# Kernel tuning notes

Hardware: AMD Instinct MI355X
Metric: run time of the kernel (lower is better)

Reference implementation:

```python
import jax, jax.numpy as jnp
import numpy as np

N = 50000        # nodes
E = 800000       # edges
D_IN = 512       # input_shape
PROJ = 256       # proj_dim
H = 4            # num_heads
C = 32           # hidden_channels
HC = H * C
NUM_LABELS = 10
SLOPE = 0.2      # GATv2 LeakyReLU negative slope


def _glorot(key, shape):
    fan_in = shape[-1]
    return jax.random.normal(key, shape, jnp.float32) / jnp.sqrt(jnp.float32(fan_in))


def setup_inputs() -> dict:
    key = jax.random.key(0)
    ks = jax.random.split(key, 16)
    inp = {}
    inp["x"] = jax.random.normal(ks[0], (N, D_IN), jnp.float32)
    inp["edge_index"] = jax.random.randint(ks[1], (2, E), 0, N, dtype=jnp.int64)
    # projection Linear
    inp["W_proj"] = _glorot(ks[2], (PROJ, D_IN)); inp["b_proj"] = jnp.zeros((PROJ,), jnp.float32)
    # GATv2 layer 1: lin_l, lin_r, att, bias
    inp["Wl1"] = _glorot(ks[3], (HC, PROJ)); inp["bl1"] = jnp.zeros((HC,), jnp.float32)
    inp["Wr1"] = _glorot(ks[4], (HC, PROJ)); inp["br1"] = jnp.zeros((HC,), jnp.float32)
    inp["att1"] = _glorot(ks[5], (H, C)); inp["bias1"] = jnp.zeros((HC,), jnp.float32)
    # GATv2 layer 2
    inp["Wl2"] = _glorot(ks[6], (HC, HC)); inp["bl2"] = jnp.zeros((HC,), jnp.float32)
    inp["Wr2"] = _glorot(ks[7], (HC, HC)); inp["br2"] = jnp.zeros((HC,), jnp.float32)
    inp["att2"] = _glorot(ks[8], (H, C)); inp["bias2"] = jnp.zeros((HC,), jnp.float32)
    # head MLP
    inp["W1"] = _glorot(ks[9], (C, HC)); inp["b1"] = jnp.zeros((C,), jnp.float32)
    inp["W2"] = _glorot(ks[10], (NUM_LABELS, C)); inp["b2"] = jnp.zeros((NUM_LABELS,), jnp.float32)
    return inp


def _gatv2(x, src, dst, Wl, bl, Wr, br, att, bias):
    # x: [N, F_in]; src/dst: [E]. PyG GATv2Conv, concat=True, no self-loops, eval (no dropout).
    xl = (x @ Wl.T + bl).reshape(N, H, C)   # source transform
    xr = (x @ Wr.T + br).reshape(N, H, C)   # target transform
    e = jax.nn.leaky_relu(xl[src] + xr[dst], negative_slope=SLOPE)  # [E,H,C]
    logit = jnp.einsum('ehc,hc->eh', e, att)                        # [E,H]
    # segment softmax over incoming edges of each destination node
    m = jax.ops.segment_max(logit, dst, num_segments=N)             # [N,H]
    m = jnp.where(jnp.isfinite(m), m, jnp.float32(0))               # empty segments -> 0
    p = jnp.exp(logit - m[dst])                                     # [E,H]
    s = jax.ops.segment_sum(p, dst, num_segments=N)                 # [N,H]
    alpha = p / (s[dst] + jnp.float32(1e-16))                       # [E,H]
    out = jax.ops.segment_sum(xl[src] * alpha[:, :, None], dst, num_segments=N)  # [N,H,C]
    return out.reshape(N, HC) + bias


def reference(x, edge_index, W_proj, b_proj, Wl1, bl1, Wr1, br1, att1, bias1,
              Wl2, bl2, Wr2, br2, att2, bias2, W1, b1, W2, b2):
    src, dst = edge_index[0], edge_index[1]
    h = jax.nn.elu(x @ W_proj.T + b_proj)
    h = jax.nn.elu(_gatv2(h, src, dst, Wl1, bl1, Wr1, br1, att1, bias1))
    h = jax.nn.elu(_gatv2(h, src, dst, Wl2, bl2, Wr2, br2, att2, bias2))
    h = jax.nn.elu(h @ W1.T + b1)
    return h @ W2.T + b2
```

## Files before the change

### kernel.cpp

```cpp
#include <hip/hip_runtime.h>
#include <cstdint>
#include <cstddef>

constexpr int NN = 50000;
constexpr int NE = 800000;

typedef _Float16 half8 __attribute__((ext_vector_type(8)));
typedef _Float16 half4v __attribute__((ext_vector_type(4)));
typedef _Float16 half2v __attribute__((ext_vector_type(2)));
typedef float f32x16 __attribute__((ext_vector_type(16)));
typedef unsigned short ushort_t;

__device__ inline ushort_t f2h(float f) {
  _Float16 h = (_Float16)f;
  return __builtin_bit_cast(ushort_t, h);
}

#if __has_builtin(__builtin_amdgcn_fdot2)
__device__ inline float fdot2(half2v a, half2v b, float c) {
  return __builtin_amdgcn_fdot2(a, b, c, false);
}
#else
__device__ inline float fdot2(half2v a, half2v b, float c) {
  return c + (float)a[0] * (float)b[0] + (float)a[1] * (float)b[1];
}
#endif

__global__ void k_wconv(const float* __restrict__ W, ushort_t* __restrict__ Bh,
                        int M, int K, int total) {
  int idx = blockIdx.x * 256 + threadIdx.x;
  if (idx >= total) return;
  int j = idx & 7;
  int l = (idx >> 3) & 63;
  int blk = idx >> 9;
  int nKB = K >> 4;
  int cb = blk / nKB, kb = blk - cb * nKB;
  int col = cb * 32 + (l & 31);
  int k = kb * 16 + ((l >> 5) & 1) * 8 + j;
  float v = (col < M) ? W[(size_t)col * K + k] : 0.f;
  Bh[idx] = f2h(v);
}

template<int ACT, int OUTMODE, int BKT, int AFP16, int NCB>
__global__ __launch_bounds__(512) void gemm_mfma(const void* __restrict__ Av,
    const ushort_t* __restrict__ Bh,
    const float* __restrict__ bias, const float* __restrict__ bias2,
    float* __restrict__ C, ushort_t* __restrict__ C16a,
    ushort_t* __restrict__ C16b, int N, int M, int K)
{
  constexpr int NKK = BKT / 16;
  __shared__ ushort_t Ah[2][2 * NKK * 512];
  const int t = threadIdx.x;
  const int lane = t & 63;
  const int wid = t >> 6;
  const int wr = wid >> 2;
  const int wc = wid & 3;
  const int row0 = blockIdx.x * 64;
  const int col0 = blockIdx.y * (128 * NCB);
  const int nKB = K >> 4;
  const int nK = K / BKT;
  const int cb0 = (col0 >> 5) + wc * NCB;

  int s_r, s_k, sb0, sb1 = 0;
  bool ok0 = false, ok1 = false;
  if constexpr (!AFP16) {
    s_r = t >> 4; s_k = (t & 15) * 4;
    sb0 = (s_k >> 4) * 512 + (s_r + 32 * ((s_k >> 3) & 1)) * 8 + (s_k & 7);
    sb1 = sb0 + NKK * 512;
    ok0 = (row0 + s_r) < N;
    ok1 = (row0 + s_r + 32) < N;
  } else if constexpr (BKT == 64) {
    s_r = t >> 3; s_k = (t & 7) * 8;
    sb0 = ((s_r >> 5) * NKK + (s_k >> 4)) * 512 +
          ((s_r & 31) + 32 * ((s_k >> 3) & 1)) * 8;
    ok0 = (row0 + s_r) < N;
  } else {
    s_r = t >> 3; s_k = (t & 7) * 4;
    sb0 = ((s_r >> 5) * NKK + (s_k >> 4)) * 512 +
          ((s_r & 31) + 32 * ((s_k >> 3) & 1)) * 8 + (s_k & 7);
    ok0 = (row0 + s_r) < N;
  }
  const float*    ap0 = (const float*)Av + (size_t)(row0 + s_r) * K + s_k;
  const float*    ap1 = (const float*)Av + (size_t)(row0 + s_r + 32) * K + s_k;
  const ushort_t* aph = (const ushort_t*)Av + (size_t)(row0 + s_r) * K + s_k;

  f32x16 acc0 = {}, acc1 = {};
  float4 f00 = make_float4(0, 0, 0, 0), f10 = make_float4(0, 0, 0, 0);
  float4 f01 = make_float4(0, 0, 0, 0), f11 = make_float4(0, 0, 0, 0);
  half8 h8 = {};
  half4v h4 = {};

  auto aload = [&](int ks) {
    if constexpr (!AFP16) {
      f00 = make_float4(0, 0, 0, 0); f10 = make_float4(0, 0, 0, 0);
      if constexpr (BKT == 128) { f01 = make_float4(0, 0, 0, 0); f11 = make_float4(0, 0, 0, 0); }
      if (ok0) {
        f00 = *(const float4*)(ap0 + (size_t)ks * BKT);
        if constexpr (BKT == 128) f01 = *(const float4*)(ap0 + (size_t)ks * BKT + 64);
      }
      if (ok1) {
        f10 = *(const float4*)(ap1 + (size_t)ks * BKT);
        if constexpr (BKT == 128) f11 = *(const float4*)(ap1 + (size_t)ks * BKT + 64);
      }
    } else if constexpr (BKT == 64) {
      half8 z = {};
      h8 = ok0 ? *(const half8*)(aph + (size_t)ks * BKT) : z;
    } else {
      half4v z = {};
      h4 = ok0 ? *(const half4v*)(aph + (size_t)ks * BKT) : z;
    }
  };
  auto cvt4 = [](float4 f) {
    half4v h;
    h[0] = (_Float16)f.x; h[1] = (_Float16)f.y;
    h[2] = (_Float16)f.z; h[3] = (_Float16)f.w;
    return h;
  };
  auto stage_write = [&](int buf) {
    if constexpr (!AFP16) {
      *(half4v*)&Ah[buf][sb0] = cvt4(f00);
      *(half4v*)&Ah[buf][sb1] = cvt4(f10);
      if constexpr (BKT == 128) {
        *(half4v*)&Ah[buf][sb0 + 2048] = cvt4(f01);
        *(half4v*)&Ah[buf][sb1 + 2048] = cvt4(f11);
      }
    } else if constexpr (BKT == 64) {
      *(half8*)&Ah[buf][sb0] = h8;
    } else {
      *(half4v*)&Ah[buf][sb0] = h4;
    }
  };

  aload(0);
  stage_write(0);
  __syncthreads();

  for (int ks = 0; ks < nK; ++ks) {
    const int cur = ks & 1;
    const int nxt = cur ^ 1;
    const bool have_next = (ks + 1 < nK);
    if (have_next) aload(ks + 1);

    #pragma unroll
    for (int kk = 0; kk < NKK; ++kk) {
      const int kbg = ks * NKK + kk;
      half8 ah = *(const half8*)&Ah[cur][(wr * NKK + kk) * 512 + lane * 8];
      const size_t bo0 = ((size_t)(cb0 * nKB + kbg) * 64 + lane) * 8;
      half8 bh0 = *(const half8*)(Bh + bo0);
      acc0 = __builtin_amdgcn_mfma_f32_32x32x16_f16(ah, bh0, acc0, 0, 0, 0);
      if constexpr (NCB == 2) {
        const size_t bo1 = ((size_t)((cb0 + 1) * nKB + kbg) * 64 + lane) * 8;
        half8 bh1 = *(const half8*)(Bh + bo1);
        acc1 = __builtin_amdgcn_mfma_f32_32x32x16_f16(ah, bh1, acc1, 0, 0, 0);
      }
    }

    if (have_next) stage_write(nxt);
    __syncthreads();
  }

  auto epi = [&](const f32x16& acc, int cb) {
    int cc = cb * 32 + (lane & 31);
    float bv;
    if constexpr (OUTMODE == 3) bv = (cc < 128) ? bias[cc] : bias2[cc - 128];
    else                        bv = (cc < M) ? bias[cc] : 0.f;
    #pragma unroll
    for (int r = 0; r < 16; ++r) {
      int rr = row0 + wr * 32 + (r & 3) + 8 * (r >> 2) + 4 * (lane >> 5);
      if (rr < N && cc < M) {
        float v = acc[r] + bv;
        if (ACT) v = v > 0.f ? v : (__expf(v) - 1.f);
        if constexpr (OUTMODE == 0)      C[(size_t)rr * M + cc] = v;
        else if constexpr (OUTMODE == 1) C16a[(size_t)rr * M + cc] = f2h(v);
        else {
          if (cc < 128) C16a[(size_t)rr * 128 + cc] = f2h(v);
          else          C16b[(size_t)rr * 128 + (cc - 128)] = f2h(v);
        }
      }
    }
  };
  epi(acc0, cb0);
  if constexpr (NCB == 2) epi(acc1, cb0 + 1);
}

__global__ void k_degrank(const int* __restrict__ ei, int* __restrict__ deg,
                          int* __restrict__ rank) {
  int e = blockIdx.x * 256 + threadIdx.x;
  if (e >= NE) return;
  int d = ei[NE + e];
  rank[e] = atomicAdd(&deg[d], 1);
}

__global__ __launch_bounds__(256) void k_scan1(const int* __restrict__ deg,
    int* __restrict__ rowstart, int* __restrict__ blocksum) {
  __shared__ int sm[256];
  int b = blockIdx.x, t = threadIdx.x;
  int i = b * 256 + t;
  int v = (i < NN) ? deg[i] : 0;
  sm[t] = v;
  __syncthreads();
  #pragma unroll
  for (int off = 1; off < 256; off <<= 1) {
    int u = (t >= off) ? sm[t - off] : 0;
    __syncthreads();
    sm[t] += u;
    __syncthreads();
  }
  if (i < NN) rowstart[i + 1] = sm[t];
  if (t == 255) blocksum[b] = sm[255];
}

__global__ __launch_bounds__(256) void k_scan2(int* __restrict__ blocksum, int nb) {
  __shared__ int sm[256];
  int t = threadIdx.x;
  int v = (t < nb) ? blocksum[t] : 0;
  sm[t] = v;
  __syncthreads();
  #pragma unroll
  for (int off = 1; off < 256; off <<= 1) {
    int u = (t >= off) ? sm[t - off] : 0;
    __syncthreads();
    sm[t] += u;
    __syncthreads();
  }
  if (t < nb) blocksum[t] = (t == 0) ? 0 : sm[t - 1];
}

__global__ __launch_bounds__(256) void k_scan3(int* __restrict__ rowstart,
    const int* __restrict__ blocksum) {
  int b = blockIdx.x, t = threadIdx.x;
  int i = b * 256 + t;
  if (i == 0) rowstart[0] = 0;
  if (i < NN) rowstart[i + 1] += blocksum[b];
}

__global__ void k_scatter(const int* __restrict__ ei, const int* __restrict__ rowstart,
                          const int* __restrict__ rank, int* __restrict__ srcp) {
  int e = blockIdx.x * 256 + threadIdx.x;
  if (e >= NE) return;
  int d = ei[NE + e];
  srcp[rowstart[d] + rank[e]] = ei[e];
}

__global__ __launch_bounds__(256) void k_gat(const ushort_t* __restrict__ xl,
    const ushort_t* __restrict__ xr, const int* __restrict__ srcp,
    const int* __restrict__ rowstart, const float* __restrict__ att,
    const float* __restrict__ bias, ushort_t* __restrict__ out)
{
  const int g = threadIdx.x >> 5;
  const int c = threadIdx.x & 31;
  const int n = blockIdx.x * 8 + g;
  const int r0 = rowstart[n], r1 = rowstart[n + 1];
  half4v xrh = *(const half4v*)(xr + (size_t)n * 128 + 4 * c);
  const half2v xr01 = {xrh[0], xrh[1]};
  const half2v xr23 = {xrh[2], xrh[3]};
  const float4 atv = *(const float4*)(att + 4 * c);
  const half2v at01 = {(_Float16)atv.x, (_Float16)atv.y};
  const half2v at23 = {(_Float16)atv.z, (_Float16)atv.w};
  const half2v k02 = {(_Float16)0.2f, (_Float16)0.2f};

  float m = -1e30f, ssum = 0.f;
  float a0 = 0.f, a1 = 0.f, a2 = 0.f, a3 = 0.f;

  auto lg = [&](int s, float4& xs) -> float {
    half4v hv = *(const half4v*)(xl + (size_t)s * 128 + 4 * c);
    xs.x = (float)hv[0]; xs.y = (float)hv[1];
    xs.z = (float)hv[2]; xs.w = (float)hv[3];
    half2v u01 = half2v{hv[0], hv[1]} + xr01;
    half2v u23 = half2v{hv[2], hv[3]} + xr23;
    u01 = __builtin_elementwise_max(u01, u01 * k02);
    u23 = __builtin_elementwise_max(u23, u23 * k02);
    float l = fdot2(u01, at01, fdot2(u23, at23, 0.f));
    l += __shfl_xor(l, 1);
    l += __shfl_xor(l, 2);
    l += __shfl_xor(l, 4);
    return l;
  };

  int j = r0;
  for (; j + 8 <= r1; j += 8) {
    int s0 = srcp[j],     s1 = srcp[j + 1], s2 = srcp[j + 2], s3 = srcp[j + 3];
    int s4 = srcp[j + 4], s5 = srcp[j + 5], s6 = srcp[j + 6], s7 = srcp[j + 7];
    float4 x0, x1, x2, x3, x4, x5, x6, x7;
    float l0 = lg(s0, x0), l1 = lg(s1, x1), l2 = lg(s2, x2), l3 = lg(s3, x3);
    float l4 = lg(s4, x4), l5 = lg(s5, x5), l6 = lg(s6, x6), l7 = lg(s7, x7);
    float mloc = fmaxf(fmaxf(fmaxf(l0, l1), fmaxf(l2, l3)),
                       fmaxf(fmaxf(l4, l5), fmaxf(l6, l7)));
    float mn = fmaxf(m, mloc);
    float sc = __expf(m - mn);
    float p0 = __expf(l0 - mn), p1 = __expf(l1 - mn);
    float p2 = __expf(l2 - mn), p3 = __expf(l3 - mn);
    float p4 = __expf(l4 - mn), p5 = __expf(l5 - mn);
    float p6 = __expf(l6 - mn), p7 = __expf(l7 - mn);
    ssum = ssum * sc + (((p0 + p1) + (p2 + p3)) + ((p4 + p5) + (p6 + p7)));
    a0 = a0 * sc + (((p0 * x0.x + p1 * x1.x) + (p2 * x2.x + p3 * x3.x)) +
                    ((p4 * x4.x + p5 * x5.x) + (p6 * x6.x + p7 * x7.x)));
    a1 = a1 * sc + (((p0 * x0.y + p1 * x1.y) + (p2 * x2.y + p3 * x3.y)) +
                    ((p4 * x4.y + p5 * x5.y) + (p6 * x6.y + p7 * x7.y)));
    a2 = a2 * sc + (((p0 * x0.z + p1 * x1.z) + (p2 * x2.z + p3 * x3.z)) +
                    ((p4 * x4.z + p5 * x5.z) + (p6 * x6.z + p7 * x7.z)));
    a3 = a3 * sc + (((p0 * x0.w + p1 * x1.w) + (p2 * x2.w + p3 * x3.w)) +
                    ((p4 * x4.w + p5 * x5.w) + (p6 * x6.w + p7 * x7.w)));
    m = mn;
  }
  for (; j + 4 <= r1; j += 4) {
    int s0 = srcp[j], s1 = srcp[j + 1], s2 = srcp[j + 2], s3 = srcp[j + 3];
    float4 x0, x1, x2, x3;
    float l0 = lg(s0, x0), l1 = lg(s1, x1), l2 = lg(s2, x2), l3 = lg(s3, x3);
    float mloc = fmaxf(fmaxf(l0, l1), fmaxf(l2, l3));
    float mn = fmaxf(m, mloc);
    float sc = __expf(m - mn);
    float p0 = __expf(l0 - mn), p1 = __expf(l1 - mn);
    float p2 = __expf(l2 - mn), p3 = __expf(l3 - mn);
    ssum = ssum * sc + ((p0 + p1) + (p2 + p3));
    a0 = a0 * sc + (p0 * x0.x + p1 * x1.x) + (p2 * x2.x + p3 * x3.x);
    a1 = a1 * sc + (p0 * x0.y + p1 * x1.y) + (p2 * x2.y + p3 * x3.y);
    a2 = a2 * sc + (p0 * x0.z + p1 * x1.z) + (p2 * x2.z + p3 * x3.z);
    a3 = a3 * sc + (p0 * x0.w + p1 * x1.w) + (p2 * x2.w + p3 * x3.w);
    m = mn;
  }
  for (; j < r1; ++j) {
    float4 xs;
    float l = lg(srcp[j], xs);
    float mn = fmaxf(m, l);
    float sc = __expf(m - mn);
    float p = __expf(l - mn);
    ssum = ssum * sc + p;
    a0 = a0 * sc + p * xs.x;
    a1 = a1 * sc + p * xs.y;
    a2 = a2 * sc + p * xs.z;
    a3 = a3 * sc + p * xs.w;
    m = mn;
  }

  const float4 bv = *(const float4*)(bias + 4 * c);
  float rinv = 1.f / (ssum + 1e-16f);
  float o0 = a0 * rinv + bv.x;
  float o1 = a1 * rinv + bv.y;
  float o2 = a2 * rinv + bv.z;
  float o3 = a3 * rinv + bv.w;
  o0 = o0 > 0.f ? o0 : (__expf(o0) - 1.f);
  o1 = o1 > 0.f ? o1 : (__expf(o1) - 1.f);
  o2 = o2 > 0.f ? o2 : (__expf(o2) - 1.f);
  o3 = o3 > 0.f ? o3 : (__expf(o3) - 1.f);
  half4v ov;
  ov[0] = (_Float16)o0; ov[1] = (_Float16)o1;
  ov[2] = (_Float16)o2; ov[3] = (_Float16)o3;
  *(half4v*)(out + (size_t)n * 128 + 4 * c) = ov;
}

__global__ void k_report_ws(float* out, int out_size, float wsz) {
  int i = blockIdx.x * 256 + threadIdx.x;
  if (i < out_size) out[i] = (i == 0) ? wsz : 0.f;
}

extern "C" void kernel_launch(void* const* d_in, const int* in_sizes, int n_in,
                              void* d_out, int out_size, void* d_ws, size_t ws_size,
                              hipStream_t stream)
{
  const float* x    = (const float*)d_in[0];
  const int*   ei   = (const int*)d_in[1];
  const float* Wp   = (const float*)d_in[2];  const float* bp    = (const float*)d_in[3];
  const float* Wl1  = (const float*)d_in[4];  const float* bl1   = (const float*)d_in[5];
  const float* Wr1  = (const float*)d_in[6];  const float* br1   = (const float*)d_in[7];
  const float* att1 = (const float*)d_in[8];  const float* bias1 = (const float*)d_in[9];
  const float* Wl2  = (const float*)d_in[10]; const float* bl2   = (const float*)d_in[11];
  const float* Wr2  = (const float*)d_in[12]; const float* br2   = (const float*)d_in[13];
  const float* att2 = (const float*)d_in[14]; const float* bias2 = (const float*)d_in[15];
  const float* W1   = (const float*)d_in[16]; const float* b1    = (const float*)d_in[17];
  const float* W2   = (const float*)d_in[18]; const float* b2    = (const float*)d_in[19];
  float* out = (float*)d_out;

  constexpr size_t NEED = 122300000;
  if (ws_size < NEED) {
    k_report_ws<<<(out_size + 255) / 256, 256, 0, stream>>>(out, out_size, (float)ws_size);
    return;
  }
  char* ws = (char*)d_ws;
  ushort_t* h0h   = (ushort_t*)(ws + 0);
  ushort_t* h1h   = h0h;
  ushort_t* h2h   = (ushort_t*)(ws + 25600000);
  ushort_t* xlh   = (ushort_t*)(ws + 51200000);
  ushort_t* xrh   = (ushort_t*)(ws + 76800000);
  ushort_t* h3h   = (ushort_t*)(ws + 102400000);
  ushort_t* wb    = (ushort_t*)(ws + 108800000);
  int*      srcp  = (int*)(ws + 115200000);
  int*      rank  = (int*)(ws + 118400000);
  int*      deg   = (int*)(ws + 121600000);
  int*      rowst = (int*)(ws + 122000000);
  int*      bsum  = (int*)(ws + 122250000);

  ushort_t* Wph  = wb;
  ushort_t* WB1h = wb + 131072;
  ushort_t* WB2h = wb + 196608;
  ushort_t* W1h  = wb + 229376;
  ushort_t* W2h  = wb + 233472;

  hipMemsetAsync(deg, 0, NN * sizeof(int), stream);

  k_wconv<<<(131072+255)/256, 256, 0, stream>>>(Wp,  Wph,          256, 512, 131072);
  k_wconv<<<(32768+255)/256,  256, 0, stream>>>(Wl1, WB1h,         128, 256, 32768);
  k_wconv<<<(32768+255)/256,  256, 0, stream>>>(Wr1, WB1h + 32768, 128, 256, 32768);
  k_wconv<<<(16384+255)/256,  256, 0, stream>>>(Wl2, WB2h,         128, 128, 16384);
  k_wconv<<<(16384+255)/256,  256, 0, stream>>>(Wr2, WB2h + 16384, 128, 128, 16384);
  k_wconv<<<(4096+255)/256,   256, 0, stream>>>(W1,  W1h,          32,  128, 4096);
  k_wconv<<<(1024+255)/256,   256, 0, stream>>>(W2,  W2h,          10,  32,  1024);

  constexpr int NB = (NN + 255) / 256;
  k_degrank<<<(NE+255)/256, 256, 0, stream>>>(ei, deg, rank);
  k_scan1  <<<NB, 256, 0, stream>>>(deg, rowst, bsum);
  k_scan2  <<<1, 256, 0, stream>>>(bsum, NB);
  k_scan3  <<<NB, 256, 0, stream>>>(rowst, bsum);
  k_scatter<<<(NE+255)/256, 256, 0, stream>>>(ei, rowst, rank, srcp);

  constexpr int GX = (NN + 63) / 64;

  gemm_mfma<1,1,128,0,2><<<dim3(GX, 1), 512, 0, stream>>>(
      x, Wph, bp, nullptr, nullptr, h0h, nullptr, NN, 256, 512);

  gemm_mfma<0,3,64,1,2><<<dim3(GX, 1), 512, 0, stream>>>(
      h0h, WB1h, bl1, br1, nullptr, xlh, xrh, NN, 256, 256);
  k_gat<<<NN/8, 256, 0, stream>>>(xlh, xrh, srcp, rowst, att1, bias1, h1h);

  gemm_mfma<0,3,64,1,2><<<dim3(GX, 1), 512, 0, stream>>>(
      h1h, WB2h, bl2, br2, nullptr, xlh, xrh, NN, 256, 128);
  k_gat<<<NN/8, 256, 0, stream>>>(xlh, xrh, srcp, rowst, att2, bias2, h2h);

  gemm_mfma<1,1,64,1,1><<<dim3(GX, 1), 512, 0, stream>>>(
      h2h, W1h, b1, nullptr, nullptr, h3h, nullptr, NN, 32, 128);
  gemm_mfma<0,0,32,1,1><<<dim3(GX, 1), 512, 0, stream>>>(
      h3h, W2h, b2, nullptr, out, nullptr, nullptr, NN, 10, 32);
}
```

Before: 266.2 us.

## Deepen GEMM A-tile prefetch to two stages ahead with ping-pong registers

Restructures the MFMA GEMM main loop so that global loads of the A tile run two k-steps ahead, using two register sets (A and B) and an unrolled-by-two loop that alternates LDS buffers. The projection GEMM also switches from a 128-wide to a 64-wide K tile, since the BKT==128 staging path was dropped. The goal is to hide more global-load latency behind MFMA work. The cost is more live registers and more loop iterations for the projection GEMM.

```diff
diff --git a/kernel.cpp b/kernel.cpp
--- a/kernel.cpp
+++ b/kernel.cpp
@@ -85,29 +85,39 @@
   const ushort_t* aph = (const ushort_t*)Av + (size_t)(row0 + s_r) * K + s_k;
 
   f32x16 acc0 = {}, acc1 = {};
-  float4 f00 = make_float4(0, 0, 0, 0), f10 = make_float4(0, 0, 0, 0);
-  float4 f01 = make_float4(0, 0, 0, 0), f11 = make_float4(0, 0, 0, 0);
-  half8 h8 = {};
-  half4v h4 = {};
-
-  auto aload = [&](int ks) {
+  float4 fA0 = make_float4(0,0,0,0), fA1 = make_float4(0,0,0,0);
+  float4 fB0 = make_float4(0,0,0,0), fB1 = make_float4(0,0,0,0);
+  half8 hA = {}, hB = {};
+  half4v hA4 = {}, hB4 = {};
+
+  auto aloadA = [&](int ks) {
     if constexpr (!AFP16) {
-      f00 = make_float4(0, 0, 0, 0); f10 = make_float4(0, 0, 0, 0);
-      if constexpr (BKT == 128) { f01 = make_float4(0, 0, 0, 0); f11 = make_float4(0, 0, 0, 0); }
-      if (ok0) {
-        f00 = *(const float4*)(ap0 + (size_t)ks * BKT);
-        if constexpr (BKT == 128) f01 = *(const float4*)(ap0 + (size_t)ks * BKT + 64);
-      }
-      if (ok1) {
-        f10 = *(const float4*)(ap1 + (size_t)ks * BKT);
-        if constexpr (BKT == 128) f11 = *(const float4*)(ap1 + (size_t)ks * BKT + 64);
+      fA0 = make_float4(0,0,0,0); fA1 = make_float4(0,0,0,0);
+      if (ks < nK) {
+        if (ok0) fA0 = *(const float4*)(ap0 + (size_t)ks * BKT);
+        if (ok1) fA1 = *(const float4*)(ap1 + (size_t)ks * BKT);
       }
     } else if constexpr (BKT == 64) {
       half8 z = {};
-      h8 = ok0 ? *(const half8*)(aph + (size_t)ks * BKT) : z;
+      hA = (ks < nK && ok0) ? *(const half8*)(aph + (size_t)ks * BKT) : z;
     } else {
       half4v z = {};
-      h4 = ok0 ? *(const half4v*)(aph + (size_t)ks * BKT) : z;
+      hA4 = (ks < nK && ok0) ? *(const half4v*)(aph + (size_t)ks * BKT) : z;
+    }
+  };
+  auto aloadB = [&](int ks) {
+    if constexpr (!AFP16) {
+      fB0 = make_float4(0,0,0,0); fB1 = make_float4(0,0,0,0);
+      if (ks < nK) {
+        if (ok0) fB0 = *(const float4*)(ap0 + (size_t)ks * BKT);
+        if (ok1) fB1 = *(const float4*)(ap1 + (size_t)ks * BKT);
+      }
+    } else if constexpr (BKT == 64) {
+      half8 z = {};
+      hB = (ks < nK && ok0) ? *(const half8*)(aph + (size_t)ks * BKT) : z;
+    } else {
+      half4v z = {};
+      hB4 = (ks < nK && ok0) ? *(const half4v*)(aph + (size_t)ks * BKT) : z;
     }
   };
   auto cvt4 = [](float4 f) {
@@ -116,35 +126,31 @@
     h[2] = (_Float16)f.z; h[3] = (_Float16)f.w;
     return h;
   };
-  auto stage_write = [&](int buf) {
+  auto stageA = [&](int buf) {
     if constexpr (!AFP16) {
-      *(half4v*)&Ah[buf][sb0] = cvt4(f00);
-      *(half4v*)&Ah[buf][sb1] = cvt4(f10);
-      if constexpr (BKT == 128) {
-        *(half4v*)&Ah[buf][sb0 + 2048] = cvt4(f01);
-        *(half4v*)&Ah[buf][sb1 + 2048] = cvt4(f11);
-      }
+      *(half4v*)&Ah[buf][sb0] = cvt4(fA0);
+      *(half4v*)&Ah[buf][sb1] = cvt4(fA1);
     } else if constexpr (BKT == 64) {
-      *(half8*)&Ah[buf][sb0] = h8;
+      *(half8*)&Ah[buf][sb0] = hA;
     } else {
-      *(half4v*)&Ah[buf][sb0] = h4;
-    }
-  };
-
-  aload(0);
-  stage_write(0);
-  __syncthreads();
-
-  for (int ks = 0; ks < nK; ++ks) {
-    const int cur = ks & 1;
-    const int nxt = cur ^ 1;
-    const bool have_next = (ks + 1 < nK);
-    if (have_next) aload(ks + 1);
-
+      *(half4v*)&Ah[buf][sb0] = hA4;
+    }
+  };
+  auto stageB = [&](int buf) {
+    if constexpr (!AFP16) {
+      *(half4v*)&Ah[buf][sb0] = cvt4(fB0);
+      *(half4v*)&Ah[buf][sb1] = cvt4(fB1);
+    } else if constexpr (BKT == 64) {
+      *(half8*)&Ah[buf][sb0] = hB;
+    } else {
+      *(half4v*)&Ah[buf][sb0] = hB4;
+    }
+  };
+  auto mfma_step = [&](int buf, int ks) {
     #pragma unroll
     for (int kk = 0; kk < NKK; ++kk) {
       const int kbg = ks * NKK + kk;
-      half8 ah = *(const half8*)&Ah[cur][(wr * NKK + kk) * 512 + lane * 8];
+      half8 ah = *(const half8*)&Ah[buf][(wr * NKK + kk) * 512 + lane * 8];
       const size_t bo0 = ((size_t)(cb0 * nKB + kbg) * 64 + lane) * 8;
       half8 bh0 = *(const half8*)(Bh + bo0);
       acc0 = __builtin_amdgcn_mfma_f32_32x32x16_f16(ah, bh0, acc0, 0, 0, 0);
@@ -154,9 +160,25 @@
         acc1 = __builtin_amdgcn_mfma_f32_32x32x16_f16(ah, bh1, acc1, 0, 0, 0);
       }
     }
-
-    if (have_next) stage_write(nxt);
+  };
+
+  aloadA(0);
+  stageA(0);
+  aloadA(1);
+  aloadB(2);
+  __syncthreads();
+
+  for (int ks = 0; ks < nK; ks += 2) {
+    mfma_step(0, ks);
+    if (ks + 1 < nK) stageA(1);
+    aloadA(ks + 3);
     __syncthreads();
+    if (ks + 1 < nK) {
+      mfma_step(1, ks + 1);
+      if (ks + 2 < nK) stageB(0);
+      aloadB(ks + 4);
+      __syncthreads();
+    }
   }
 
   auto epi = [&](const f32x16& acc, int cb) {
@@ -415,7 +437,7 @@
 
   constexpr int GX = (NN + 63) / 64;
 
-  gemm_mfma<1,1,128,0,2><<<dim3(GX, 1), 512, 0, stream>>>(
+  gemm_mfma<1,1,64,0,2><<<dim3(GX, 1), 512, 0, stream>>>(
       x, Wph, bp, nullptr, nullptr, h0h, nullptr, NN, 256, 512);
 
   gemm_mfma<0,3,64,1,2><<<dim3(GX, 1), 512, 0, stream>>>(
```

After: 277.5 us. 4.2% more time.
